# Performance work log

Hardware: AMD Instinct MI355X
Metric: run time of the kernel (lower is better)

## Reference

```python
import jax, jax.numpy as jnp
import numpy as np

D_MODEL = 1024
NUM_HEADS = 16
D_K = D_MODEL // NUM_HEADS
D_FF = 4096


def setup_inputs() -> dict:
    key = jax.random.key(0)
    ks = jax.random.split(key, 12)
    s = 1.0 / np.sqrt(D_MODEL)
    sf = 1.0 / np.sqrt(D_FF)
    return {
        "x": jax.random.normal(ks[0], (2, 2048, D_MODEL), dtype=jnp.float32),
        # nn.Linear weights are [out_features, in_features]
        "Wq": jax.random.uniform(ks[1], (D_MODEL, D_MODEL), jnp.float32, -s, s),
        "Wk": jax.random.uniform(ks[2], (D_MODEL, D_MODEL), jnp.float32, -s, s),
        "Wv": jax.random.uniform(ks[3], (D_MODEL, D_MODEL), jnp.float32, -s, s),
        "Wo": jax.random.uniform(ks[4], (D_MODEL, D_MODEL), jnp.float32, -s, s),
        "W1": jax.random.uniform(ks[5], (D_FF, D_MODEL), jnp.float32, -s, s),
        "W2": jax.random.uniform(ks[6], (D_MODEL, D_FF), jnp.float32, -sf, sf),
        "g1": jnp.ones((D_MODEL,), jnp.float32),
        "b1": jnp.zeros((D_MODEL,), jnp.float32),
        "g2": jnp.ones((D_MODEL,), jnp.float32),
        "b2": jnp.zeros((D_MODEL,), jnp.float32),
    }


def _layer_norm(x, gamma, beta, eps=1e-5):
    mu = jnp.mean(x, axis=-1, keepdims=True)
    var = jnp.mean((x - mu) ** 2, axis=-1, keepdims=True)
    return (x - mu) * jax.lax.rsqrt(var + eps) * gamma + beta


def reference(x, Wq, Wk, Wv, Wo, W1, W2, g1, b1, g2, b2):
    B, S, _ = x.shape
    H, Dk = NUM_HEADS, D_K
    # projections (Linear: x @ W.T), split heads -> [B, H, S, Dk]
    q = (x @ Wq.T).reshape(B, S, H, Dk).transpose(0, 2, 1, 3)
    k = (x @ Wk.T).reshape(B, S, H, Dk).transpose(0, 2, 1, 3)
    v = (x @ Wv.T).reshape(B, S, H, Dk).transpose(0, 2, 1, 3)
    scores = jnp.einsum('bhsd,bhtd->bhst', q, k) / jnp.sqrt(jnp.float32(Dk))
    attn = jax.nn.softmax(scores, axis=-1)
    out = jnp.einsum('bhst,bhtd->bhsd', attn, v)
    out = out.transpose(0, 2, 1, 3).reshape(B, S, H * Dk)
    out = out @ Wo.T
    x_after_attn = _layer_norm(x + out, g1, b1)
    ff = jax.nn.gelu(x_after_attn @ W1.T, approximate=False)
    ff_out = ff @ W2.T
    return _layer_norm(x_after_attn + ff_out, g2, b2)
```

## Files before the change

kernel.cpp:

```cpp
#include <hip/hip_runtime.h>
#include <hip/hip_bf16.h>
#include <cstdint>
#include <cstddef>

#define D_MODEL 1024
#define D_FF    4096
#define NTOK    4096
#define SEQ     2048
#define NH      16
#define DK      64
#define LDQ     3072

typedef __bf16 bf16;
typedef __bf16 bf16_8 __attribute__((ext_vector_type(8)));
typedef __bf16 bf16_4 __attribute__((ext_vector_type(4)));
typedef float  f32_4  __attribute__((ext_vector_type(4)));

__device__ __forceinline__ void async_copy16(const bf16* g, bf16* l) {
    __builtin_amdgcn_global_load_lds((const __attribute__((address_space(1))) void*)g,
                                     (__attribute__((address_space(3))) void*)l,
                                     16, 0, 0);
}

__global__ __launch_bounds__(256)
void cast_all(const float* __restrict__ x,  const float* __restrict__ Wq,
              const float* __restrict__ Wk, const float* __restrict__ Wv,
              const float* __restrict__ Wo, const float* __restrict__ W1,
              const float* __restrict__ W2,
              bf16* __restrict__ xb, bf16* __restrict__ Wqkvb,
              bf16* __restrict__ Wob, bf16* __restrict__ W1b,
              bf16* __restrict__ W2b) {
    const int blk = blockIdx.x;
    const float* s; bf16* d; int off;
    if (blk < 4096)       { s = x;  d = xb;              off = blk; }
    else if (blk < 5120)  { s = Wq; d = Wqkvb;           off = blk - 4096; }
    else if (blk < 6144)  { s = Wk; d = Wqkvb + 1048576; off = blk - 5120; }
    else if (blk < 7168)  { s = Wv; d = Wqkvb + 2097152; off = blk - 6144; }
    else if (blk < 8192)  { s = Wo; d = Wob;             off = blk - 7168; }
    else if (blk < 12288) { s = W1; d = W1b;             off = blk - 8192; }
    else                  { s = W2; d = W2b;             off = blk - 12288; }
    const int i = off * 1024 + threadIdx.x * 4;
    float4 v = *(const float4*)(s + i);
    bf16_4 o;
    o[0] = (bf16)v.x; o[1] = (bf16)v.y; o[2] = (bf16)v.z; o[3] = (bf16)v.w;
    *(bf16_4*)(d + i) = o;
}

template <int EPI>
__global__ __launch_bounds__(256, 2)
void gemm_bt(const bf16* __restrict__ A, const bf16* __restrict__ B,
             bf16* __restrict__ C0, size_t cstride, bf16* __restrict__ Vt,
             int M, int N, int ldk, int kLen) {
    __shared__ bf16 As[128 * 64];
    __shared__ bf16 Bs[128 * 64];
    const int tid  = threadIdx.x;
    const int wave = tid >> 6, lane = tid & 63;
    const int quad = lane >> 4, l15 = lane & 15;
    const int wm = wave >> 1, wn = wave & 1;
    const int bm = blockIdx.x, bn = blockIdx.y, z = blockIdx.z;

    const bf16* A0 = A + (size_t)bm * 128 * ldk + (size_t)z * kLen;
    const bf16* B0 = B + (size_t)bn * 128 * ldk + (size_t)z * kLen;

    f32_4 acc[4][4];
#pragma unroll
    for (int i = 0; i < 4; i++)
#pragma unroll
        for (int j = 0; j < 4; j++) acc[i][j] = (f32_4){0.f, 0.f, 0.f, 0.f};

    const int srow8 = lane >> 3;
    const int slog  = (lane & 7) ^ srow8;
    const int rx    = l15 & 7;

    for (int k0 = 0; k0 < kLen; k0 += 64) {
#pragma unroll
        for (int c = 0; c < 4; c++) {
            int row = c * 32 + wave * 8 + srow8;
            async_copy16(&A0[(size_t)row * ldk + k0 + slog * 8],
                         &As[(c * 32 + wave * 8) * 64]);
        }
#pragma unroll
        for (int c = 0; c < 4; c++) {
            int row = c * 32 + wave * 8 + srow8;
            async_copy16(&B0[(size_t)row * ldk + k0 + slog * 8],
                         &Bs[(c * 32 + wave * 8) * 64]);
        }
        __syncthreads();

#pragma unroll
        for (int kh = 0; kh < 2; kh++) {
            bf16_8 af[4], bfr[4];
#pragma unroll
            for (int mi = 0; mi < 4; mi++)
                af[mi] = *(const bf16_8*)&As[(wm * 64 + mi * 16 + l15) * 64 +
                                             (((kh * 4 + quad) ^ rx) * 8)];
#pragma unroll
            for (int ni = 0; ni < 4; ni++)
                bfr[ni] = *(const bf16_8*)&Bs[(wn * 64 + ni * 16 + l15) * 64 +
                                              (((kh * 4 + quad) ^ rx) * 8)];
#pragma unroll
            for (int mi = 0; mi < 4; mi++)
#pragma unroll
                for (int ni = 0; ni < 4; ni++)
                    acc[mi][ni] = __builtin_amdgcn_mfma_f32_16x16x32_bf16(
                        af[mi], bfr[ni], acc[mi][ni], 0, 0, 0);
        }
        __syncthreads();
    }

    bf16* C = C0 + (size_t)z * cstride;
    const int row0 = bm * 128 + wm * 64 + quad * 4;
    const int col0 = bn * 128 + wn * 64 + l15;

    if (EPI == 3 && bn >= 16) {
        const int bvt = bm >> 4;
#pragma unroll
        for (int mi = 0; mi < 4; mi++) {
            const int srow = (row0 + mi * 16) & 2047;
#pragma unroll
            for (int ni = 0; ni < 4; ni++) {
                const int ch = col0 + ni * 16 - 2048;
                bf16_4 w;
#pragma unroll
                for (int r = 0; r < 4; r++) w[r] = (bf16)acc[mi][ni][r];
                *(bf16_4*)&Vt[((size_t)(bvt * 1024 + ch)) * SEQ + srow] = w;
            }
        }
        return;
    }

#pragma unroll
    for (int mi = 0; mi < 4; mi++) {
#pragma unroll
        for (int ni = 0; ni < 4; ni++) {
#pragma unroll
            for (int r = 0; r < 4; r++) {
                int row = row0 + mi * 16 + r;
                int col = col0 + ni * 16;
                size_t idx = (size_t)row * N + col;
                float v = acc[mi][ni][r];
                if (EPI == 2) {
                    float g = 0.5f * v * (1.0f + erff(v * 0.70710678118654752f));
                    C[idx] = (bf16)g;
                } else {
                    C[idx] = (bf16)v;
                }
            }
        }
    }
}

__global__ __launch_bounds__(256)
void attn7(const bf16* __restrict__ QKV, const bf16* __restrict__ Vt,
           bf16* __restrict__ O) {
    __shared__ bf16 Ks[2][64 * 64];
    __shared__ bf16 Vs[2][64 * 64];

    const int tid  = threadIdx.x;
    const int wave = tid >> 6, lane = tid & 63;
    const int quad = lane >> 4, l15 = lane & 15;
    const int qb = blockIdx.x & 31;
    const int h  = (blockIdx.x >> 5) & 15;
    const int b  = blockIdx.x >> 9;

    const bf16* Qg = QKV + (size_t)(b * SEQ) * LDQ + h * 64;
    const bf16* Kg = QKV + (size_t)(b * SEQ) * LDQ + 1024 + h * 64;
    const bf16* Vg = Vt + (size_t)(b * 1024 + h * 64) * SEQ;

    const int qrow = qb * 64 + wave * 16 + l15;
    const bf16_8 qf0 = *(const bf16_8*)&Qg[(size_t)qrow * LDQ + quad * 8];
    const bf16_8 qf1 = *(const bf16_8*)&Qg[(size_t)qrow * LDQ + 32 + quad * 8];

    const int m0 = wave * 8 + (lane >> 3);
    const int sg = lane & 7;
    const int sw = m0 & 7;
    const int xl = l15 & 7;
    const int fr = ((m0 >> 4) << 5) | ((m0 & 12) << 1) | (m0 & 3);

    bf16_8 one8;
#pragma unroll
    for (int i = 0; i < 8; i++) one8[i] = (bf16)1.0f;

    f32_4 lacc = (f32_4){0.f, 0.f, 0.f, 0.f};
    f32_4 o_acc[4];
#pragma unroll
    for (int d = 0; d < 4; d++) o_acc[d] = (f32_4){0.f, 0.f, 0.f, 0.f};

    async_copy16(&Kg[(size_t)fr * LDQ + ((sg ^ sw) * 8)], &Ks[0][wave * 512]);
    async_copy16(&Kg[(size_t)(fr + 4) * LDQ + ((sg ^ sw) * 8)],
                 &Ks[0][2048 + wave * 512]);
    async_copy16(&Vg[(size_t)m0 * SEQ + ((sg ^ sw) * 8)], &Vs[0][wave * 512]);
    async_copy16(&Vg[(size_t)(m0 + 32) * SEQ + ((sg ^ sw) * 8)],
                 &Vs[0][2048 + wave * 512]);
    __syncthreads();

    for (int t = 0; t < SEQ / 64; ++t) {
        const int cur = t & 1;
        if (t + 1 < SEQ / 64) {
            const int k1 = (t + 1) * 64;
            bf16* kd = Ks[cur ^ 1];
            bf16* vd = Vs[cur ^ 1];
            async_copy16(&Kg[(size_t)(k1 + fr) * LDQ + ((sg ^ sw) * 8)],
                         kd + wave * 512);
            async_copy16(&Kg[(size_t)(k1 + fr + 4) * LDQ + ((sg ^ sw) * 8)],
                         kd + 2048 + wave * 512);
            async_copy16(&Vg[(size_t)m0 * SEQ + k1 + ((sg ^ sw) * 8)],
                         vd + wave * 512);
            async_copy16(&Vg[(size_t)(m0 + 32) * SEQ + k1 + ((sg ^ sw) * 8)],
                         vd + 2048 + wave * 512);
        }

        const bf16* KsC = Ks[cur];
        const bf16* VsC = Vs[cur];

        f32_4 s[4];
#pragma unroll
        for (int ni = 0; ni < 4; ni++) {
            const bf16* kp = &KsC[(ni * 16 + l15) * 64];
            bf16_8 kb0 = *(const bf16_8*)&kp[(quad ^ xl) * 8];
            bf16_8 kb1 = *(const bf16_8*)&kp[((quad + 4) ^ xl) * 8];
            f32_4 zz = (f32_4){0.f, 0.f, 0.f, 0.f};
            zz = __builtin_amdgcn_mfma_f32_16x16x32_bf16(kb0, qf0, zz, 0, 0, 0);
            s[ni] = __builtin_amdgcn_mfma_f32_16x16x32_bf16(kb1, qf1, zz, 0, 0, 0);
        }

        bf16_8 pf0, pf1;
#pragma unroll
        for (int ni = 0; ni < 4; ni++) {
#pragma unroll
            for (int r = 0; r < 4; r++) {
                float p = __expf(fmaf(s[ni][r], 0.125f, -8.0f));
                bf16 pb = (bf16)p;
                const int jx = ((ni >> 1) << 2) + r;
                if ((ni & 1) == 0) pf0[jx] = pb;
                else               pf1[jx] = pb;
            }
        }

        lacc = __builtin_amdgcn_mfma_f32_16x16x32_bf16(one8, pf0, lacc, 0, 0, 0);
        lacc = __builtin_amdgcn_mfma_f32_16x16x32_bf16(one8, pf1, lacc, 0, 0, 0);

#pragma unroll
        for (int dt = 0; dt < 4; dt++) {
            const bf16* vp = &VsC[(dt * 16 + l15) * 64];
            bf16_8 vb0 = *(const bf16_8*)&vp[(quad ^ xl) * 8];
            bf16_8 vb1 = *(const bf16_8*)&vp[((quad + 4) ^ xl) * 8];
            o_acc[dt] = __builtin_amdgcn_mfma_f32_16x16x32_bf16(vb0, pf0, o_acc[dt], 0, 0, 0);
            o_acc[dt] = __builtin_amdgcn_mfma_f32_16x16x32_bf16(vb1, pf1, o_acc[dt], 0, 0, 0);
        }

        __syncthreads();
    }

    const float rl = 1.0f / lacc[0];

    bf16* P = (bf16*)Ks + wave * 1280;
#pragma unroll
    for (int dt = 0; dt < 4; dt++) {
        bf16_4 pk;
#pragma unroll
        for (int r = 0; r < 4; r++) pk[r] = (bf16)(o_acc[dt][r] * rl);
        int G = dt * 2 + (quad >> 1);
        *(bf16_4*)&P[l15 * 80 + ((G ^ xl) * 8) + ((quad & 1) * 4)] = pk;
    }
    const int q2 = lane >> 2, dc = lane & 3, x2 = q2 & 7;
    bf16_8 o0 = *(const bf16_8*)&P[q2 * 80 + (((dc * 2) ^ x2) * 8)];
    bf16_8 o1 = *(const bf16_8*)&P[q2 * 80 + (((dc * 2 + 1) ^ x2) * 8)];
    const size_t row = (size_t)b * SEQ + qb * 64 + wave * 16 + q2;
    *(bf16_8*)&O[row * D_MODEL + h * 64 + dc * 16] = o0;
    *(bf16_8*)&O[row * D_MODEL + h * 64 + dc * 16 + 8] = o1;
}

template <bool A32, bool O32>
__global__ __launch_bounds__(256)
void ln_kernel(const void* __restrict__ av, const bf16* __restrict__ p0,
               const bf16* __restrict__ p1, const bf16* __restrict__ p2,
               const bf16* __restrict__ p3,
               const float* __restrict__ gamma, const float* __restrict__ beta,
               void* __restrict__ yv) {
    const int row = blockIdx.x;
    const int tid = threadIdx.x;
    const size_t off = (size_t)row * D_MODEL;
    float v[4];
    {
        bf16_4 a0 = *(const bf16_4*)(p0 + off + tid * 4);
        bf16_4 a1 = *(const bf16_4*)(p1 + off + tid * 4);
        bf16_4 a2 = *(const bf16_4*)(p2 + off + tid * 4);
        bf16_4 a3 = *(const bf16_4*)(p3 + off + tid * 4);
        if (A32) {
            float4 xa = *(const float4*)((const float*)av + off + tid * 4);
            v[0] = xa.x; v[1] = xa.y; v[2] = xa.z; v[3] = xa.w;
        } else {
            bf16_4 xa = *(const bf16_4*)((const bf16*)av + off + tid * 4);
#pragma unroll
            for (int i = 0; i < 4; i++) v[i] = (float)xa[i];
        }
#pragma unroll
        for (int i = 0; i < 4; i++)
            v[i] += ((float)a0[i] + (float)a1[i]) + ((float)a2[i] + (float)a3[i]);
    }
    float s = v[0] + v[1] + v[2] + v[3];
    float ss = v[0] * v[0] + v[1] * v[1] + v[2] * v[2] + v[3] * v[3];
#pragma unroll
    for (int m = 1; m < 64; m <<= 1) {
        s  += __shfl_xor(s, m);
        ss += __shfl_xor(ss, m);
    }
    __shared__ float red_s[4], red_q[4];
    int wave = tid >> 6, lane = tid & 63;
    if (lane == 0) { red_s[wave] = s; red_q[wave] = ss; }
    __syncthreads();
    s  = red_s[0] + red_s[1] + red_s[2] + red_s[3];
    ss = red_q[0] + red_q[1] + red_q[2] + red_q[3];
    float mu   = s * (1.f / D_MODEL);
    float var  = ss * (1.f / D_MODEL) - mu * mu;
    float rstd = rsqrtf(var + 1e-5f);
    float4 gg = *(const float4*)(gamma + tid * 4);
    float4 be = *(const float4*)(beta + tid * 4);
    float y0 = (v[0] - mu) * rstd * gg.x + be.x;
    float y1 = (v[1] - mu) * rstd * gg.y + be.y;
    float y2 = (v[2] - mu) * rstd * gg.z + be.z;
    float y3 = (v[3] - mu) * rstd * gg.w + be.w;
    if (O32) {
        *(float4*)((float*)yv + off + tid * 4) = make_float4(y0, y1, y2, y3);
    } else {
        bf16_4 o;
        o[0] = (bf16)y0; o[1] = (bf16)y1; o[2] = (bf16)y2; o[3] = (bf16)y3;
        *(bf16_4*)((bf16*)yv + off + tid * 4) = o;
    }
}

extern "C" void kernel_launch(void* const* d_in, const int* in_sizes, int n_in,
                              void* d_out, int out_size, void* d_ws, size_t ws_size,
                              hipStream_t stream) {
    (void)in_sizes; (void)n_in; (void)out_size; (void)ws_size;
    const float* x  = (const float*)d_in[0];
    const float* Wq = (const float*)d_in[1];
    const float* Wk = (const float*)d_in[2];
    const float* Wv = (const float*)d_in[3];
    const float* Wo = (const float*)d_in[4];
    const float* W1 = (const float*)d_in[5];
    const float* W2 = (const float*)d_in[6];
    const float* g1 = (const float*)d_in[7];
    const float* b1 = (const float*)d_in[8];
    const float* g2 = (const float*)d_in[9];
    const float* b2 = (const float*)d_in[10];

    char* ws = (char*)d_ws;
    bf16*  xb    = (bf16*)(ws + 0);
    bf16*  aob   = xb;
    bf16*  ln1b  = (bf16*)(ws + 0);
    bf16*  QKVb  = (bf16*)(ws + 8388608);
    bf16*  Vtb   = (bf16*)(ws + 33554432);
    bf16*  hb    = (bf16*)(ws + 8388608);
    bf16*  Wqkvb = (bf16*)(ws + 41943040);
    bf16*  Wob   = (bf16*)(ws + 48234496);
    bf16*  W1b   = (bf16*)(ws + 50331648);
    bf16*  W2b   = (bf16*)(ws + 58720256);
    bf16*  proj0 = (bf16*)(ws + 67108864);
    const size_t PSTRIDE = (size_t)NTOK * D_MODEL;

    cast_all<<<dim3(16384), 256, 0, stream>>>(x, Wq, Wk, Wv, Wo, W1, W2,
                                              xb, Wqkvb, Wob, W1b, W2b);

    gemm_bt<3><<<dim3(NTOK / 128, 3072 / 128, 1), 256, 0, stream>>>(
        xb, Wqkvb, QKVb, 0, Vtb, NTOK, 3072, D_MODEL, D_MODEL);

    attn7<<<dim3(1024), 256, 0, stream>>>(QKVb, Vtb, aob);

    gemm_bt<0><<<dim3(NTOK / 128, D_MODEL / 128, 4), 256, 0, stream>>>(
        aob, Wob, proj0, PSTRIDE, nullptr, NTOK, D_MODEL, D_MODEL, 256);
    ln_kernel<true, false><<<NTOK, 256, 0, stream>>>(
        x, proj0, proj0 + PSTRIDE, proj0 + 2 * PSTRIDE, proj0 + 3 * PSTRIDE,
        g1, b1, ln1b);

    gemm_bt<2><<<dim3(NTOK / 128, D_FF / 128, 1), 256, 0, stream>>>(
        ln1b, W1b, hb, 0, nullptr, NTOK, D_FF, D_MODEL, D_MODEL);

    gemm_bt<0><<<dim3(NTOK / 128, D_MODEL / 128, 4), 256, 0, stream>>>(
        hb, W2b, proj0, PSTRIDE, nullptr, NTOK, D_MODEL, D_FF, 1024);
    ln_kernel<false, true><<<NTOK, 256, 0, stream>>>(
        ln1b, proj0, proj0 + PSTRIDE, proj0 + 2 * PSTRIDE, proj0 + 3 * PSTRIDE,
        g2, b2, d_out);
}
```

Baseline: 323.4 us.

## Widen attention blocks to 128 query rows sharing each K/V tile

The attention kernel now runs 8 waves per block covering 128 query rows instead of 4 waves covering 64. Each K/V tile loaded into shared memory is reused by twice as many queries, which halves global K/V traffic and halves the per-thread async copy count. In exchange the grid drops to 512 blocks, which may reduce occupancy or load balance across CUs, and the larger blocks make synchronisation barriers more costly.

```diff
diff --git a/kernel.cpp b/kernel.cpp
--- a/kernel.cpp
+++ b/kernel.cpp
@@ -150,24 +150,23 @@
     }
 }
 
-__global__ __launch_bounds__(256)
-void attn7(const bf16* __restrict__ QKV, const bf16* __restrict__ Vt,
+__global__ __launch_bounds__(512)
+void attn8(const bf16* __restrict__ QKV, const bf16* __restrict__ Vt,
            bf16* __restrict__ O) {
-    __shared__ bf16 Ks[2][64 * 64];
-    __shared__ bf16 Vs[2][64 * 64];
+    __shared__ bf16 SM[2][8192];
 
     const int tid  = threadIdx.x;
     const int wave = tid >> 6, lane = tid & 63;
     const int quad = lane >> 4, l15 = lane & 15;
-    const int qb = blockIdx.x & 31;
-    const int h  = (blockIdx.x >> 5) & 15;
-    const int b  = blockIdx.x >> 9;
+    const int qb = blockIdx.x & 15;
+    const int h  = (blockIdx.x >> 4) & 15;
+    const int b  = blockIdx.x >> 8;
 
     const bf16* Qg = QKV + (size_t)(b * SEQ) * LDQ + h * 64;
     const bf16* Kg = QKV + (size_t)(b * SEQ) * LDQ + 1024 + h * 64;
     const bf16* Vg = Vt + (size_t)(b * 1024 + h * 64) * SEQ;
 
-    const int qrow = qb * 64 + wave * 16 + l15;
+    const int qrow = qb * 128 + wave * 16 + l15;
     const bf16_8 qf0 = *(const bf16_8*)&Qg[(size_t)qrow * LDQ + quad * 8];
     const bf16_8 qf1 = *(const bf16_8*)&Qg[(size_t)qrow * LDQ + 32 + quad * 8];
 
@@ -175,7 +174,8 @@
     const int sg = lane & 7;
     const int sw = m0 & 7;
     const int xl = l15 & 7;
-    const int fr = ((m0 >> 4) << 5) | ((m0 & 12) << 1) | (m0 & 3);
+    const int fr = (((m0 >> 4) & 1) << 5) | ((m0 & 12) << 1) |
+                   (((m0 >> 5) & 1) << 2) | (m0 & 3);
 
     bf16_8 one8;
 #pragma unroll
@@ -186,32 +186,24 @@
 #pragma unroll
     for (int d = 0; d < 4; d++) o_acc[d] = (f32_4){0.f, 0.f, 0.f, 0.f};
 
-    async_copy16(&Kg[(size_t)fr * LDQ + ((sg ^ sw) * 8)], &Ks[0][wave * 512]);
-    async_copy16(&Kg[(size_t)(fr + 4) * LDQ + ((sg ^ sw) * 8)],
-                 &Ks[0][2048 + wave * 512]);
-    async_copy16(&Vg[(size_t)m0 * SEQ + ((sg ^ sw) * 8)], &Vs[0][wave * 512]);
-    async_copy16(&Vg[(size_t)(m0 + 32) * SEQ + ((sg ^ sw) * 8)],
-                 &Vs[0][2048 + wave * 512]);
+    async_copy16(&Kg[(size_t)fr * LDQ + ((sg ^ sw) * 8)],
+                 &SM[0][wave * 512]);
+    async_copy16(&Vg[(size_t)m0 * SEQ + ((sg ^ sw) * 8)],
+                 &SM[0][4096 + wave * 512]);
     __syncthreads();
 
     for (int t = 0; t < SEQ / 64; ++t) {
         const int cur = t & 1;
         if (t + 1 < SEQ / 64) {
             const int k1 = (t + 1) * 64;
-            bf16* kd = Ks[cur ^ 1];
-            bf16* vd = Vs[cur ^ 1];
             async_copy16(&Kg[(size_t)(k1 + fr) * LDQ + ((sg ^ sw) * 8)],
-                         kd + wave * 512);
-            async_copy16(&Kg[(size_t)(k1 + fr + 4) * LDQ + ((sg ^ sw) * 8)],
-                         kd + 2048 + wave * 512);
+                         &SM[cur ^ 1][wave * 512]);
             async_copy16(&Vg[(size_t)m0 * SEQ + k1 + ((sg ^ sw) * 8)],
-                         vd + wave * 512);
-            async_copy16(&Vg[(size_t)(m0 + 32) * SEQ + k1 + ((sg ^ sw) * 8)],
-                         vd + 2048 + wave * 512);
-        }
-
-        const bf16* KsC = Ks[cur];
-        const bf16* VsC = Vs[cur];
+                         &SM[cur ^ 1][4096 + wave * 512]);
+        }
+
+        const bf16* KsC = SM[cur];
+        const bf16* VsC = SM[cur] + 4096;
 
         f32_4 s[4];
 #pragma unroll
@@ -254,7 +246,7 @@
 
     const float rl = 1.0f / lacc[0];
 
-    bf16* P = (bf16*)Ks + wave * 1280;
+    bf16* P = (bf16*)SM + wave * 1280;
 #pragma unroll
     for (int dt = 0; dt < 4; dt++) {
         bf16_4 pk;
@@ -266,7 +258,7 @@
     const int q2 = lane >> 2, dc = lane & 3, x2 = q2 & 7;
     bf16_8 o0 = *(const bf16_8*)&P[q2 * 80 + (((dc * 2) ^ x2) * 8)];
     bf16_8 o1 = *(const bf16_8*)&P[q2 * 80 + (((dc * 2 + 1) ^ x2) * 8)];
-    const size_t row = (size_t)b * SEQ + qb * 64 + wave * 16 + q2;
+    const size_t row = (size_t)b * SEQ + qb * 128 + wave * 16 + q2;
     *(bf16_8*)&O[row * D_MODEL + h * 64 + dc * 16] = o0;
     *(bf16_8*)&O[row * D_MODEL + h * 64 + dc * 16 + 8] = o1;
 }
@@ -366,7 +358,7 @@
     gemm_bt<3><<<dim3(NTOK / 128, 3072 / 128, 1), 256, 0, stream>>>(
         xb, Wqkvb, QKVb, 0, Vtb, NTOK, 3072, D_MODEL, D_MODEL);
 
-    attn7<<<dim3(1024), 256, 0, stream>>>(QKVb, Vtb, aob);
+    attn8<<<dim3(512), 512, 0, stream>>>(QKVb, Vtb, aob);
 
     gemm_bt<0><<<dim3(NTOK / 128, D_MODEL / 128, 4), 256, 0, stream>>>(
         aob, Wob, proj0, PSTRIDE, nullptr, NTOK, D_MODEL, D_MODEL, 256);
```

New measurement: 298.2 us. 7.8% less time.
